# Performance work log

Hardware: AMD Instinct MI355X
Metric: run time of the kernel (lower is better)

The kernel has to match this reference:

```python
import jax, jax.numpy as jnp
import numpy as np

SHIFT = 1  # fixed value of the randomized shift_direction (+1)


def setup_inputs() -> dict:
    key = jax.random.key(0)
    kx, kw = jax.random.split(key)
    x = jax.random.normal(kx, (1, 128, 56, 56), dtype=jnp.float32)
    W = jax.random.normal(kw, (32, 64, 3), dtype=jnp.float32)
    return {"x": x, "W": W}


def reference(x, W):
    # channel-pair sum: (1,128,56,56) -> (1,2,64,56,56) -> sum over pair axis
    t2 = x.reshape(1, 2, 64, 56, 56).sum(axis=1)  # (1,64,56,56)
    # unfold with kernel (3,1), padding (1,0): 3-tap window along H
    xp = jnp.pad(t2, ((0, 0), (0, 0), (1, 1), (0, 0)))  # (1,64,58,56)
    # t3[l,c,k,h,w] = xp[l,c,h+k,w]
    t3 = jnp.stack([xp[:, :, k:k + 56, :] for k in range(3)], axis=2)  # (1,64,3,56,56)
    # conv-as-einsum: contract channel and tap dims with weights (32,64,3)
    out = jnp.einsum('lckhw,ick->lihw', t3, W)  # (1,32,56,56)
    # roll shift along width (dim 3)
    return jnp.roll(out, SHIFT, axis=3)
```

## Files before the change

### kernel.cpp

```cpp
#include <hip/hip_runtime.h>

#define HW 56
#define PLANE 3136
#define CH 64
#define CI 32
#define NI 2
#define NQ 4
#define CQ (CH/NQ)

__global__ __launch_bounds__(256) void convshift_kernel(
    const float* __restrict__ x, const float* __restrict__ Wt, float* __restrict__ out)
{
    __shared__ float sW[NI * CH * 3];
    __shared__ float red[NQ][NI][64];

    const int i0  = blockIdx.y * NI;
    const int tid = threadIdx.x;
    #pragma unroll
    for (int t = tid; t < NI * CH * 3; t += 256)
        sW[t] = Wt[i0 * (CH * 3) + t];
    __syncthreads();

    const int px = tid & 63;
    const int q  = tid >> 6;
    const int p  = blockIdx.x * 64 + px;
    const int h  = p / HW;
    const int w  = p - h * HW;

    const bool v0 = (h > 0), v2 = (h < HW - 1);
    const int hm = v0 ? h - 1 : 0;
    const int hp = v2 ? h + 1 : HW - 1;

    const int c0 = q * CQ;
    const float* __restrict__ xa = x + c0 * PLANE + w;
    const float* __restrict__ xb = x + (CH + c0) * PLANE + w;
    const int r0 = hm * HW, r1 = h * HW, r2 = hp * HW;

    float acc[NI][3];
    #pragma unroll
    for (int ii = 0; ii < NI; ++ii) { acc[ii][0] = 0.f; acc[ii][1] = 0.f; acc[ii][2] = 0.f; }

    float A0[2][8], A1[2][8], A2[2][8], B0[2][8], B1[2][8], B2[2][8];

    #pragma unroll
    for (int j = 0; j < 8; ++j) {
        const int o = j * PLANE;
        A0[0][j] = xa[o + r0]; A1[0][j] = xa[o + r1]; A2[0][j] = xa[o + r2];
        B0[0][j] = xb[o + r0]; B1[0][j] = xb[o + r1]; B2[0][j] = xb[o + r2];
    }

    #pragma unroll
    for (int chk = 0; chk < 2; ++chk) {
        const int cur = chk & 1, nxt = cur ^ 1;
        if (chk < 1) {
            #pragma unroll
            for (int j = 0; j < 8; ++j) {
                const int o = (8 + j) * PLANE;
                A0[nxt][j] = xa[o + r0]; A1[nxt][j] = xa[o + r1]; A2[nxt][j] = xa[o + r2];
                B0[nxt][j] = xb[o + r0]; B1[nxt][j] = xb[o + r1]; B2[nxt][j] = xb[o + r2];
            }
        }
        #pragma unroll
        for (int j = 0; j < 8; ++j) {
            const int ca = c0 + chk * 8 + j;
            const float s0 = A0[cur][j] + B0[cur][j];
            const float s1 = A1[cur][j] + B1[cur][j];
            const float s2 = A2[cur][j] + B2[cur][j];
            #pragma unroll
            for (int ii = 0; ii < NI; ++ii) {
                acc[ii][0] += s0 * sW[ii * (CH * 3) + ca * 3 + 0];
                acc[ii][1] += s1 * sW[ii * (CH * 3) + ca * 3 + 1];
                acc[ii][2] += s2 * sW[ii * (CH * 3) + ca * 3 + 2];
            }
        }
    }

    #pragma unroll
    for (int ii = 0; ii < NI; ++ii) {
        float r = acc[ii][1];
        if (v0) r += acc[ii][0];
        if (v2) r += acc[ii][2];
        red[q][ii][px] = r;
    }
    __syncthreads();

    if (tid < NI * 64) {
        const int ii  = tid >> 6;
        const int px2 = tid & 63;
        const float s = (red[0][ii][px2] + red[1][ii][px2])
                      + (red[2][ii][px2] + red[3][ii][px2]);
        const int p2 = blockIdx.x * 64 + px2;
        const int h2 = p2 / HW;
        const int w2 = p2 - h2 * HW;
        int wst = w2 + 1; if (wst == HW) wst = 0;
        out[(i0 + ii) * PLANE + h2 * HW + wst] = s;
    }
}

extern "C" void kernel_launch(void* const* d_in, const int* in_sizes, int n_in,
                              void* d_out, int out_size, void* d_ws, size_t ws_size,
                              hipStream_t stream) {
    const float* x  = (const float*)d_in[0];
    const float* Wt = (const float*)d_in[1];
    float* out = (float*)d_out;

    dim3 grid(49, CI / NI), block(256);
    hipLaunchKernelGGL(convshift_kernel, grid, block, 0, stream, x, Wt, out);
}
```

Measured before the change: 10.34 us.

## Repartition work: 32-pixel tiles, 8 channel groups, 4 outputs per block

Each block now covers 32 pixels instead of 64, 4 output channels instead of 2, and splits the 64 input channels across 8 groups of 8 instead of 4 groups of 16. The two-stage register double-buffer of loads is dropped, since each thread now handles only 8 channels in a single load batch. The grid goes from 49x16 to 98x8 blocks. The aim is more in-flight loads per output, shorter per-thread serial chains, and fewer redundant input reads across output-channel blocks, at the cost of a larger cross-group reduction in shared memory and 32-wide pixel rows that fill only half of a 64-lane wavefront.

Result: slower. 10.73 us (+3.8%).

```diff
diff --git a/kernel.cpp b/kernel.cpp
--- a/kernel.cpp
+++ b/kernel.cpp
@@ -4,15 +4,16 @@
 #define PLANE 3136
 #define CH 64
 #define CI 32
-#define NI 2
-#define NQ 4
-#define CQ (CH/NQ)
+#define NI 4
+#define NQ 8
+#define CQ 8
+#define PX 32
 
 __global__ __launch_bounds__(256) void convshift_kernel(
     const float* __restrict__ x, const float* __restrict__ Wt, float* __restrict__ out)
 {
     __shared__ float sW[NI * CH * 3];
-    __shared__ float red[NQ][NI][64];
+    __shared__ float red[NQ][NI][PX];
 
     const int i0  = blockIdx.y * NI;
     const int tid = threadIdx.x;
@@ -21,9 +22,9 @@
         sW[t] = Wt[i0 * (CH * 3) + t];
     __syncthreads();
 
-    const int px = tid & 63;
-    const int q  = tid >> 6;
-    const int p  = blockIdx.x * 64 + px;
+    const int px = tid & (PX - 1);
+    const int q  = tid >> 5;
+    const int p  = blockIdx.x * PX + px;
     const int h  = p / HW;
     const int w  = p - h * HW;
 
@@ -36,42 +37,29 @@
     const float* __restrict__ xb = x + (CH + c0) * PLANE + w;
     const int r0 = hm * HW, r1 = h * HW, r2 = hp * HW;
 
+    float A0[CQ], A1[CQ], A2[CQ], B0[CQ], B1[CQ], B2[CQ];
+    #pragma unroll
+    for (int j = 0; j < CQ; ++j) {
+        const int o = j * PLANE;
+        A0[j] = xa[o + r0]; A1[j] = xa[o + r1]; A2[j] = xa[o + r2];
+        B0[j] = xb[o + r0]; B1[j] = xb[o + r1]; B2[j] = xb[o + r2];
+    }
+
     float acc[NI][3];
     #pragma unroll
     for (int ii = 0; ii < NI; ++ii) { acc[ii][0] = 0.f; acc[ii][1] = 0.f; acc[ii][2] = 0.f; }
 
-    float A0[2][8], A1[2][8], A2[2][8], B0[2][8], B1[2][8], B2[2][8];
-
     #pragma unroll
-    for (int j = 0; j < 8; ++j) {
-        const int o = j * PLANE;
-        A0[0][j] = xa[o + r0]; A1[0][j] = xa[o + r1]; A2[0][j] = xa[o + r2];
-        B0[0][j] = xb[o + r0]; B1[0][j] = xb[o + r1]; B2[0][j] = xb[o + r2];
-    }
-
-    #pragma unroll
-    for (int chk = 0; chk < 2; ++chk) {
-        const int cur = chk & 1, nxt = cur ^ 1;
-        if (chk < 1) {
-            #pragma unroll
-            for (int j = 0; j < 8; ++j) {
-                const int o = (8 + j) * PLANE;
-                A0[nxt][j] = xa[o + r0]; A1[nxt][j] = xa[o + r1]; A2[nxt][j] = xa[o + r2];
-                B0[nxt][j] = xb[o + r0]; B1[nxt][j] = xb[o + r1]; B2[nxt][j] = xb[o + r2];
-            }
-        }
+    for (int j = 0; j < CQ; ++j) {
+        const int ca = c0 + j;
+        const float s0 = A0[j] + B0[j];
+        const float s1 = A1[j] + B1[j];
+        const float s2 = A2[j] + B2[j];
         #pragma unroll
-        for (int j = 0; j < 8; ++j) {
-            const int ca = c0 + chk * 8 + j;
-            const float s0 = A0[cur][j] + B0[cur][j];
-            const float s1 = A1[cur][j] + B1[cur][j];
-            const float s2 = A2[cur][j] + B2[cur][j];
-            #pragma unroll
-            for (int ii = 0; ii < NI; ++ii) {
-                acc[ii][0] += s0 * sW[ii * (CH * 3) + ca * 3 + 0];
-                acc[ii][1] += s1 * sW[ii * (CH * 3) + ca * 3 + 1];
-                acc[ii][2] += s2 * sW[ii * (CH * 3) + ca * 3 + 2];
-            }
+        for (int ii = 0; ii < NI; ++ii) {
+            acc[ii][0] += s0 * sW[ii * (CH * 3) + ca * 3 + 0];
+            acc[ii][1] += s1 * sW[ii * (CH * 3) + ca * 3 + 1];
+            acc[ii][2] += s2 * sW[ii * (CH * 3) + ca * 3 + 2];
         }
     }
 
@@ -84,12 +72,14 @@
     }
     __syncthreads();
 
-    if (tid < NI * 64) {
-        const int ii  = tid >> 6;
-        const int px2 = tid & 63;
-        const float s = (red[0][ii][px2] + red[1][ii][px2])
-                      + (red[2][ii][px2] + red[3][ii][px2]);
-        const int p2 = blockIdx.x * 64 + px2;
+    if (tid < NI * PX) {
+        const int ii  = tid >> 5;
+        const int px2 = tid & (PX - 1);
+        const float s = ((red[0][ii][px2] + red[1][ii][px2])
+                       + (red[2][ii][px2] + red[3][ii][px2]))
+                      + ((red[4][ii][px2] + red[5][ii][px2])
+                       + (red[6][ii][px2] + red[7][ii][px2]));
+        const int p2 = blockIdx.x * PX + px2;
         const int h2 = p2 / HW;
         const int w2 = p2 - h2 * HW;
         int wst = w2 + 1; if (wst == HW) wst = 0;
@@ -104,6 +94,6 @@
     const float* Wt = (const float*)d_in[1];
     float* out = (float*)d_out;
 
-    dim3 grid(49, CI / NI), block(256);
+    dim3 grid(98, CI / NI), block(256);
     hipLaunchKernelGGL(convshift_kernel, grid, block, 0, stream, x, Wt, out);
 }
```
